# Kernel tuning notes

Measured on AMD Instinct MI355X. Metric: run time of the kernel, lower is better.

Reference implementation:

```python
import jax, jax.numpy as jnp
import numpy as np

B, T, D = 2, 2048, 1024
H, HS = 16, 64
EPS = 1e-5

def _ln(x, g, b):
    m = jnp.mean(x, axis=-1, keepdims=True)
    v = jnp.mean((x - m) ** 2, axis=-1, keepdims=True)
    return (x - m) * jax.lax.rsqrt(v + EPS) * g + b

def setup_inputs() -> dict:
    key = jax.random.key(0)
    ks = jax.random.split(key, 8)
    s_in = 1.0 / np.sqrt(D)
    s_ff = 1.0 / np.sqrt(4 * D)
    return {
        "embds": jax.random.normal(ks[0], (B, T, D), jnp.float32),
        "Wq": jax.random.normal(ks[1], (H, D, HS), jnp.float32) * s_in,
        "Wk": jax.random.normal(ks[2], (H, D, HS), jnp.float32) * s_in,
        "Wv": jax.random.normal(ks[3], (H, D, HS), jnp.float32) * s_in,
        "ln1_g": jnp.ones((D,), jnp.float32),
        "ln1_b": jnp.zeros((D,), jnp.float32),
        "ln2_g": jnp.ones((D,), jnp.float32),
        "ln2_b": jnp.zeros((D,), jnp.float32),
        "W1": jax.random.normal(ks[4], (D, 4 * D), jnp.float32) * s_in,
        "b1": jnp.zeros((4 * D,), jnp.float32),
        "W2": jax.random.normal(ks[5], (4 * D, D), jnp.float32) * s_ff,
        "b2": jnp.zeros((D,), jnp.float32),
    }

def reference(embds, Wq, Wk, Wv, ln1_g, ln1_b, ln2_g, ln2_b, W1, b1, W2, b2):
    _, t, d = embds.shape
    x = _ln(embds, ln1_g, ln1_b)
    q = jnp.einsum("btd,hde->bhte", x, Wq)
    k = jnp.einsum("btd,hde->bhte", x, Wk)
    v = jnp.einsum("btd,hde->bhte", x, Wv)
    # NOTE: repo scales by num_embds**-0.5 (C of input), not head_size**-0.5
    scores = jnp.einsum("bhte,bhse->bhts", q, k) * (d ** -0.5)
    causal = jnp.tril(jnp.ones((t, t), bool))
    scores = jnp.where(causal, scores, -jnp.inf)
    w = jax.nn.softmax(scores, axis=-1)
    o = jnp.einsum("bhts,bhse->bhte", w, v)  # [B,H,T,HS]
    attn = o.transpose(0, 2, 1, 3).reshape(embds.shape[0], t, -1)  # concat heads
    embds = embds + attn
    y = _ln(embds, ln2_g, ln2_b)
    ff = jax.nn.relu(y @ W1 + b1) @ W2 + b2
    return embds + ff
```

## Files before the change

kernel.cpp:

```cpp
#include <hip/hip_runtime.h>

using s16x8 = __attribute__((ext_vector_type(8))) short;
using f32x4 = __attribute__((ext_vector_type(4))) float;
typedef unsigned int   u32;
typedef unsigned short u16;

__device__ __forceinline__ u16 f2bf(float f) {
  u32 u = __float_as_uint(f);
  u += 0x7fffu + ((u >> 16) & 1u);
  return (u16)(u >> 16);
}
__device__ __forceinline__ float bf2f(u16 s) {
  return __uint_as_float(((u32)s) << 16);
}

typedef __attribute__((address_space(1))) const unsigned int g_u32;
typedef __attribute__((address_space(3))) unsigned int l_u32;
__device__ __forceinline__ void gload16(const void* g, void* l) {
  __builtin_amdgcn_global_load_lds((g_u32*)g, (l_u32*)l, 16, 0, 0);
}

#define WAITB(N) asm volatile("s_waitcnt vmcnt(" #N ")\ns_barrier" ::: "memory")
#define BAR()    asm volatile("s_barrier" ::: "memory")

__device__ __forceinline__ size_t kfrag_addr(int bh, int t, int e) {
  const int pair = (((t >> 4) & 3) << 1) + (e >> 5);
  const int slot = ((e >> 3) & 3) * 16 + (t & 15);
  return ((((size_t)bh * 32 + (t >> 6)) * 8 + pair) * 64 + slot) * 8 + (e & 7);
}
__device__ __forceinline__ size_t vfrag_addr(int bh, int t, int e) {
  const int pair = (((e >> 4) & 3) << 1) + ((t >> 5) & 1);
  const int slot = ((t >> 3) & 3) * 16 + (e & 15);
  return ((((size_t)bh * 32 + (t >> 6)) * 8 + pair) * 64 + slot) * 8 + (t & 7);
}

__global__ __launch_bounds__(256) void transpose_pack(
    const float* __restrict__ src, u16* __restrict__ dst, int R, int C)
{
  __shared__ u16 tile[64][66];
  const int tid = threadIdx.x;
  const int c0 = blockIdx.x * 64, r0 = blockIdx.y * 64;
  const size_t zoff = (size_t)blockIdx.z * R * C;
  src += zoff; dst += zoff;
  const int rr = tid >> 6, cc = tid & 63;
  #pragma unroll
  for (int i = 0; i < 16; ++i)
    tile[i * 4 + rr][cc] = f2bf(src[(size_t)(r0 + i * 4 + rr) * C + c0 + cc]);
  __syncthreads();
  #pragma unroll
  for (int i = 0; i < 16; ++i)
    dst[(size_t)(c0 + i * 4 + rr) * R + r0 + cc] = tile[cc][i * 4 + rr];
}

__global__ __launch_bounds__(256) void transpose_qkv(
    const float* __restrict__ Wq, const float* __restrict__ Wk,
    const float* __restrict__ Wv, u16* __restrict__ dst)
{
  __shared__ u16 tile[64][66];
  const int tid = threadIdx.x;
  const int sel = blockIdx.z >> 4, head = blockIdx.z & 15;
  const int r0 = blockIdx.y * 64;
  const float* src = ((sel == 0) ? Wq : (sel == 1) ? Wk : Wv) + (size_t)head * 65536;
  u16* d = dst + ((size_t)sel << 20) + (size_t)head * 65536;
  const int rr = tid >> 6, cc = tid & 63;
  #pragma unroll
  for (int i = 0; i < 16; ++i)
    tile[i * 4 + rr][cc] = f2bf(src[(size_t)(r0 + i * 4 + rr) * 64 + cc]);
  __syncthreads();
  #pragma unroll
  for (int i = 0; i < 16; ++i)
    d[(size_t)(i * 4 + rr) * 1024 + r0 + cc] = tile[cc][i * 4 + rr];
}

__global__ __launch_bounds__(256) void ln_kernel(
    const float* __restrict__ x, const float* __restrict__ g,
    const float* __restrict__ be, u16* __restrict__ out)
{
  const int row = blockIdx.x, tid = threadIdx.x;
  const int lane = tid & 63, wave = tid >> 6;
  const float4 v = ((const float4*)(x + (size_t)row * 1024))[tid];
  float s  = v.x + v.y + v.z + v.w;
  float sq = v.x * v.x + v.y * v.y + v.z * v.z + v.w * v.w;
  #pragma unroll
  for (int m = 1; m < 64; m <<= 1) { s += __shfl_xor(s, m); sq += __shfl_xor(sq, m); }
  __shared__ float rs[4], rq[4];
  if (lane == 0) { rs[wave] = s; rq[wave] = sq; }
  __syncthreads();
  s  = rs[0] + rs[1] + rs[2] + rs[3];
  sq = rq[0] + rq[1] + rq[2] + rq[3];
  const float mean = s * (1.0f / 1024.0f);
  const float var  = sq * (1.0f / 1024.0f) - mean * mean;
  const float rstd = rsqrtf(var + 1e-5f);
  const int c = tid * 4;
  const float4 gv = ((const float4*)g)[tid];
  const float4 bv = ((const float4*)be)[tid];
  ushort4 o;
  o.x = f2bf((v.x - mean) * rstd * gv.x + bv.x);
  o.y = f2bf((v.y - mean) * rstd * gv.y + bv.y);
  o.z = f2bf((v.z - mean) * rstd * gv.z + bv.z);
  o.w = f2bf((v.w - mean) * rstd * gv.w + bv.w);
  *(ushort4*)&out[(size_t)row * 1024 + c] = o;
}

#define MFMA_Q(MQ, NH)                                                        \
  do {                                                                        \
    __builtin_amdgcn_s_setprio(1);                                            \
    _Pragma("unroll") for (int m_ = 0; m_ < 4; ++m_)                          \
      _Pragma("unroll") for (int n_ = 0; n_ < 2; ++n_)                        \
        _Pragma("unroll") for (int ks_ = 0; ks_ < 2; ++ks_)                   \
          acc[MQ * 4 + m_][NH * 2 + n_] =                                     \
            __builtin_amdgcn_mfma_f32_16x16x32_bf16(                          \
              aF[m_][ks_], (NH ? b1F : b0F)[n_][ks_],                         \
              acc[MQ * 4 + m_][NH * 2 + n_], 0, 0, 0);                        \
    __builtin_amdgcn_s_setprio(0);                                            \
  } while (0)

template<int MODE>
__global__ __launch_bounds__(512, 2) void gemm256(
    const u16* __restrict__ A, int lda, const u16* __restrict__ BT, int ldb,
    int K, u16* __restrict__ o1, const float* __restrict__ bias,
    u16* __restrict__ pout, u16* __restrict__ o0q, u16* __restrict__ o0k,
    u16* __restrict__ o0v)
{
  __shared__ alignas(16) u16 lds[2][2][256 * 64];
  const int tid = threadIdx.x, lane = tid & 63, w = tid >> 6;
  const int wm = w >> 2, wn = w & 3;
  const int fr = lane & 15, g = lane >> 4;
  const int gx = gridDim.x, nwg = gx * gridDim.y;
  int lid = blockIdx.y * gx + blockIdx.x;
  lid = (lid & 7) * (nwg >> 3) + (lid >> 3);
  const int col0 = (lid % gx) * 256, row0 = (lid / gx) * 256;
  const int koff = (MODE == 3) ? blockIdx.z * 1024 : 0;
  if constexpr (MODE == 3) pout += (size_t)blockIdx.z * (4096 * 1024);

  const int srow = w * 16 + (lane >> 3);
  const int scol8 = (lane & 7) ^ ((lane >> 3) & 7);
  const u16* Ab = A  + (size_t)(row0 + srow) * lda + koff + scol8 * 8;
  const u16* Bb = BT + (size_t)(col0 + srow) * ldb + koff + scol8 * 8;
  const int sdst = (w * 16) * 64 + lane * 8;

  const int x7 = fr & 7;
  const int rA = wm * 128 + fr;
  const int rB = wn * 64 + fr;

  f32x4 acc[8][4] = {};
  s16x8 aF[4][2], b0F[2][2], b1F[2][2];
  const int nkt = K >> 6;

  auto stA = [&](int buf, int half, int kt) {
    #pragma unroll
    for (int g2 = 0; g2 < 2; ++g2)
      gload16(Ab + (size_t)(half * 128 + g2 * 8) * lda + kt * 64,
              &lds[buf][0][(half * 128 + g2 * 8) * 64 + sdst]);
  };
  auto stB = [&](int buf, int half, int kt) {
    #pragma unroll
    for (int g2 = 0; g2 < 2; ++g2)
      gload16(Bb + (size_t)(half * 128 + g2 * 8) * ldb + kt * 64,
              &lds[buf][1][(half * 128 + g2 * 8) * 64 + sdst]);
  };
  auto rdA = [&](int buf, int mq) {
    #pragma unroll
    for (int m = 0; m < 4; ++m)
      #pragma unroll
      for (int ks = 0; ks < 2; ++ks)
        aF[m][ks] = *(const s16x8*)
          &lds[buf][0][(rA + mq * 64 + m * 16) * 64 + ((ks * 4 + g) ^ x7) * 8];
  };
  auto rdB0 = [&](int buf) {
    #pragma unroll
    for (int n = 0; n < 2; ++n)
      #pragma unroll
      for (int ks = 0; ks < 2; ++ks)
        b0F[n][ks] = *(const s16x8*)
          &lds[buf][1][(rB + n * 16) * 64 + ((ks * 4 + g) ^ x7) * 8];
  };
  auto rdB1 = [&](int buf) {
    #pragma unroll
    for (int n = 0; n < 2; ++n)
      #pragma unroll
      for (int ks = 0; ks < 2; ++ks)
        b1F[n][ks] = *(const s16x8*)
          &lds[buf][1][(rB + (n + 2) * 16) * 64 + ((ks * 4 + g) ^ x7) * 8];
  };

  stA(0, 0, 0); stA(0, 1, 0); stB(0, 0, 0); stB(0, 1, 0);
  stA(1, 0, 1); stA(1, 1, 1); stB(1, 0, 1); stB(1, 1, 1);
  WAITB(8);

  const int niter = nkt >> 1;
  for (int i = 0; i < niter; ++i) {
    #pragma unroll
    for (int half = 0; half < 2; ++half) {
      const int buf = half;
      const int skt = 2 * i + 2 + half;
      const bool st = (skt < nkt);
      rdA(buf, 0); rdB0(buf);
      BAR();
      MFMA_Q(0, 0);
      BAR();
      rdB1(buf);
      if (st) stB(buf, 0, skt);
      BAR();
      MFMA_Q(0, 1);
      BAR();
      rdA(buf, 1);
      if (st) stA(buf, 0, skt);
      BAR();
      MFMA_Q(1, 0);
      BAR();
      if (st) { stA(buf, 1, skt); stB(buf, 1, skt); }
      BAR();
      MFMA_Q(1, 1);
      WAITB(6);
    }
  }

  const float QSCALE = 0.03125f * 1.4426950408889634f;
  #pragma unroll
  for (int m8 = 0; m8 < 8; ++m8) {
    const int rbase = row0 + wm * 128 + m8 * 16 + g * 4;
    #pragma unroll
    for (int n4 = 0; n4 < 4; ++n4) {
      const int col = col0 + wn * 64 + n4 * 16 + fr;
      if constexpr (MODE == 0) {
        const int ww = col >> 10, h = (col >> 6) & 15, e = col & 63;
        const int b = rbase >> 11, t0 = rbase & 2047;
        const int bh = b * 16 + h;
        if (ww == 0) {
          #pragma unroll
          for (int j = 0; j < 4; ++j)
            o0q[((size_t)bh * 2048 + (t0 + j)) * 64 + e] =
              f2bf(acc[m8][n4][j] * QSCALE);
        } else if (ww == 1) {
          #pragma unroll
          for (int j = 0; j < 4; ++j)
            o0k[kfrag_addr(bh, t0 + j, e)] = f2bf(acc[m8][n4][j]);
        } else {
          ushort4 pk;
          pk.x = f2bf(acc[m8][n4][0]); pk.y = f2bf(acc[m8][n4][1]);
          pk.z = f2bf(acc[m8][n4][2]); pk.w = f2bf(acc[m8][n4][3]);
          *(ushort4*)&o0v[vfrag_addr(bh, t0, e)] = pk;
        }
      } else if constexpr (MODE == 1) {
        const float bb = bias[col];
        #pragma unroll
        for (int j = 0; j < 4; ++j)
          o1[(size_t)(rbase + j) * 4096 + col] =
            f2bf(fmaxf(acc[m8][n4][j] + bb, 0.0f));
      } else {
        #pragma unroll
        for (int j = 0; j < 4; ++j)
          pout[(size_t)(rbase + j) * 1024 + col] = f2bf(acc[m8][n4][j]);
      }
    }
  }
}

__global__ __launch_bounds__(256) void ff2_reduce(
    const u16* __restrict__ pbuf, const float* __restrict__ e2,
    const float* __restrict__ b2, float* __restrict__ out)
{
  const int i4 = blockIdx.x * 256 + threadIdx.x;
  const int row = i4 >> 8, c4 = i4 & 255;
  float4 a = ((const float4*)e2)[i4];
  const float4 bb = ((const float4*)b2)[c4];
  a.x += bb.x; a.y += bb.y; a.z += bb.z; a.w += bb.w;
  #pragma unroll
  for (int z = 0; z < 4; ++z) {
    const ushort4 p = *(const ushort4*)
      &pbuf[(size_t)z * (4096 * 1024) + (size_t)row * 1024 + c4 * 4];
    a.x += bf2f(p.x); a.y += bf2f(p.y); a.z += bf2f(p.z); a.w += bf2f(p.w);
  }
  ((float4*)out)[i4] = a;
}

__global__ __launch_bounds__(256, 2) void attn_mfma(
    const u16* __restrict__ q, const u16* __restrict__ kfragG,
    const u16* __restrict__ vfragG, const float* __restrict__ embds,
    float* __restrict__ e2)
{
  __shared__ alignas(16) u16 kbuf[2][4096];
  __shared__ alignas(16) u16 vbuf[2][4096];
  __shared__ alignas(16) u16 p_sm[8][16][68];
  const int tid = threadIdx.x, lane = tid & 63, wave = tid >> 6;
  const int bh = blockIdx.x & 31;
  const int qb = 15 - (blockIdx.x >> 5);
  const int q0 = qb * 128 + wave * 32;
  const int b = bh >> 4, h = bh & 15;
  const int fr = lane & 15, g = lane >> 4;

  s16x8 qf[2][2];
  #pragma unroll
  for (int u = 0; u < 2; ++u) {
    const u16* qp = q + ((size_t)bh * 2048 + q0 + u * 16 + fr) * 64 + g * 8;
    qf[u][0] = *(const s16x8*)(qp);
    qf[u][1] = *(const s16x8*)(qp + 32);
  }

  f32x4 o_acc[2][4] = {};
  float lacc[2][4] = {};

  const size_t fragbase = (size_t)bh * 131072;
  const int nch = qb * 2 + 2;

  auto stage_kv = [&](int sel, int c) {
    const size_t cb = fragbase + (size_t)c * 4096;
    gload16(kfragG + cb + (wave * 2 + 0) * 512 + lane * 8, &kbuf[sel][(wave * 2 + 0) * 512]);
    gload16(kfragG + cb + (wave * 2 + 1) * 512 + lane * 8, &kbuf[sel][(wave * 2 + 1) * 512]);
    gload16(vfragG + cb + (wave * 2 + 0) * 512 + lane * 8, &vbuf[sel][(wave * 2 + 0) * 512]);
    gload16(vfragG + cb + (wave * 2 + 1) * 512 + lane * 8, &vbuf[sel][(wave * 2 + 1) * 512]);
  };

  auto compute = [&](int sel, int s0) {
    s16x8 kf[4][2];
    #pragma unroll
    for (int n = 0; n < 4; ++n)
      #pragma unroll
      for (int ks = 0; ks < 2; ++ks)
        kf[n][ks] = *(const s16x8*)&kbuf[sel][(n * 2 + ks) * 512 + lane * 8];

    #pragma unroll
    for (int u = 0; u < 2; ++u) {
      const int q0u = q0 + u * 16;
      f32x4 sacc[4] = {};
      #pragma unroll
      for (int n = 0; n < 4; ++n) {
        sacc[n] = __builtin_amdgcn_mfma_f32_16x16x32_bf16(qf[u][0], kf[n][0], sacc[n], 0, 0, 0);
        sacc[n] = __builtin_amdgcn_mfma_f32_16x16x32_bf16(qf[u][1], kf[n][1], sacc[n], 0, 0, 0);
      }
      if (s0 + 63 > q0u) {
        #pragma unroll
        for (int n = 0; n < 4; ++n) {
          const int s = s0 + n * 16 + fr;
          #pragma unroll
          for (int j = 0; j < 4; ++j)
            if (s > q0u + g * 4 + j) sacc[n][j] = -1e30f;
        }
      }
      #pragma unroll
      for (int n = 0; n < 4; ++n)
        #pragma unroll
        for (int j = 0; j < 4; ++j) {
          const float pe = __builtin_amdgcn_exp2f(sacc[n][j]);
          lacc[u][j] += pe;
          p_sm[wave * 2 + u][g * 4 + j][n * 16 + fr] = f2bf(pe);
        }
    }

    s16x8 vf[4][2];
    #pragma unroll
    for (int n = 0; n < 4; ++n)
      #pragma unroll
      for (int ks = 0; ks < 2; ++ks)
        vf[n][ks] = *(const s16x8*)&vbuf[sel][(n * 2 + ks) * 512 + lane * 8];

    #pragma unroll
    for (int u = 0; u < 2; ++u) {
      const s16x8 pf0 = *(const s16x8*)&p_sm[wave * 2 + u][fr][g * 8];
      const s16x8 pf1 = *(const s16x8*)&p_sm[wave * 2 + u][fr][32 + g * 8];
      #pragma unroll
      for (int n = 0; n < 4; ++n) {
        o_acc[u][n] = __builtin_amdgcn_mfma_f32_16x16x32_bf16(pf0, vf[n][0], o_acc[u][n], 0, 0, 0);
        o_acc[u][n] = __builtin_amdgcn_mfma_f32_16x16x32_bf16(pf1, vf[n][1], o_acc[u][n], 0, 0, 0);
      }
    }
  };

  stage_kv(0, 0);
  for (int t = 0; t < nch; ++t) {
    WAITB(0);
    if (t + 1 < nch) stage_kv((t + 1) & 1, t + 1);
    compute(t & 1, t * 64);
  }

  #pragma unroll
  for (int u = 0; u < 2; ++u)
    #pragma unroll
    for (int j = 0; j < 4; ++j) {
      #pragma unroll
      for (int mm = 1; mm < 16; mm <<= 1) lacc[u][j] += __shfl_xor(lacc[u][j], mm);
    }

  #pragma unroll
  for (int u = 0; u < 2; ++u)
    #pragma unroll
    for (int n = 0; n < 4; ++n) {
      #pragma unroll
      for (int j = 0; j < 4; ++j) {
        const int t = q0 + u * 16 + g * 4 + j;
        const size_t oi = ((size_t)b * 2048 + t) * 1024 + (size_t)h * 64 + n * 16 + fr;
        e2[oi] = embds[oi] + o_acc[u][n][j] / lacc[u][j];
      }
    }
}

extern "C" void kernel_launch(void* const* d_in, const int* in_sizes, int n_in,
                              void* d_out, int out_size, void* d_ws, size_t ws_size,
                              hipStream_t stream) {
  const float* embds = (const float*)d_in[0];
  const float* Wq    = (const float*)d_in[1];
  const float* Wk    = (const float*)d_in[2];
  const float* Wv    = (const float*)d_in[3];
  const float* ln1g  = (const float*)d_in[4];
  const float* ln1b  = (const float*)d_in[5];
  const float* ln2g  = (const float*)d_in[6];
  const float* ln2b  = (const float*)d_in[7];
  const float* W1    = (const float*)d_in[8];
  const float* b1    = (const float*)d_in[9];
  const float* W2    = (const float*)d_in[10];
  const float* b2    = (const float*)d_in[11];
  float* out = (float*)d_out;

  char* ws = (char*)d_ws;
  u16*   xln   = (u16*)(ws);
  u16*   pbuf  = (u16*)(ws);
  u16*   wqkvT = (u16*)(ws + (8ull  << 20));
  u16*   qbuf  = (u16*)(ws + (14ull << 20));
  u16*   kfrag = (u16*)(ws + (22ull << 20));
  u16*   vfrag = (u16*)(ws + (30ull << 20));
  float* e2    = (float*)(ws + (38ull << 20));
  u16*   ybuf  = (u16*)(ws + (54ull << 20));
  u16*   w1T   = (u16*)(ws + (62ull << 20));
  u16*   w2T   = (u16*)(ws + (70ull << 20));
  u16*   hid   = (u16*)(ws + (78ull << 20));

  transpose_qkv<<<dim3(1, 16, 48), 256, 0, stream>>>(Wq, Wk, Wv, wqkvT);
  transpose_pack<<<dim3(64, 16, 1), 256, 0, stream>>>(W1, w1T, 1024, 4096);
  transpose_pack<<<dim3(16, 64, 1), 256, 0, stream>>>(W2, w2T, 4096, 1024);
  ln_kernel<<<4096, 256, 0, stream>>>(embds, ln1g, ln1b, xln);
  gemm256<0><<<dim3(12, 16), 512, 0, stream>>>(xln, 1024, wqkvT, 1024, 1024,
      nullptr, nullptr, nullptr, qbuf, kfrag, vfrag);
  attn_mfma<<<512, 256, 0, stream>>>(qbuf, kfrag, vfrag, embds, e2);
  ln_kernel<<<4096, 256, 0, stream>>>(e2, ln2g, ln2b, ybuf);
  gemm256<1><<<dim3(16, 16), 512, 0, stream>>>(ybuf, 1024, w1T, 1024, 1024,
      hid, b1, nullptr, nullptr, nullptr, nullptr);
  gemm256<3><<<dim3(4, 16, 4), 512, 0, stream>>>(hid, 4096, w2T, 4096, 1024,
      nullptr, nullptr, pbuf, nullptr, nullptr, nullptr);
  ff2_reduce<<<4096, 256, 0, stream>>>(pbuf, e2, b2, out);
}
```

Measured before the change: 196.7 us.

## Load K/V fragments directly into registers with register double-buffering

```diff
diff --git a/kernel.cpp b/kernel.cpp
--- a/kernel.cpp
+++ b/kernel.cpp
@@ -280,9 +280,7 @@
     const u16* __restrict__ vfragG, const float* __restrict__ embds,
     float* __restrict__ e2)
 {
-  __shared__ alignas(16) u16 kbuf[2][4096];
-  __shared__ alignas(16) u16 vbuf[2][4096];
-  __shared__ alignas(16) u16 p_sm[8][16][68];
+  __shared__ alignas(16) u16 p_sm[4][16][68];
   const int tid = threadIdx.x, lane = tid & 63, wave = tid >> 6;
   const int bh = blockIdx.x & 31;
   const int qb = 15 - (blockIdx.x >> 5);
@@ -302,32 +300,29 @@
   float lacc[2][4] = {};
 
   const size_t fragbase = (size_t)bh * 131072;
+  const u16* kb = kfragG + fragbase + lane * 8;
+  const u16* vb = vfragG + fragbase + lane * 8;
   const int nch = qb * 2 + 2;
 
-  auto stage_kv = [&](int sel, int c) {
-    const size_t cb = fragbase + (size_t)c * 4096;
-    gload16(kfragG + cb + (wave * 2 + 0) * 512 + lane * 8, &kbuf[sel][(wave * 2 + 0) * 512]);
-    gload16(kfragG + cb + (wave * 2 + 1) * 512 + lane * 8, &kbuf[sel][(wave * 2 + 1) * 512]);
-    gload16(vfragG + cb + (wave * 2 + 0) * 512 + lane * 8, &vbuf[sel][(wave * 2 + 0) * 512]);
-    gload16(vfragG + cb + (wave * 2 + 1) * 512 + lane * 8, &vbuf[sel][(wave * 2 + 1) * 512]);
-  };
-
-  auto compute = [&](int sel, int s0) {
-    s16x8 kf[4][2];
-    #pragma unroll
-    for (int n = 0; n < 4; ++n)
-      #pragma unroll
-      for (int ks = 0; ks < 2; ++ks)
-        kf[n][ks] = *(const s16x8*)&kbuf[sel][(n * 2 + ks) * 512 + lane * 8];
-
+  auto loadKV = [&](s16x8 (&kd)[8], s16x8 (&vd)[8], int c) {
+    const u16* kc = kb + (size_t)c * 4096;
+    const u16* vc = vb + (size_t)c * 4096;
+    #pragma unroll
+    for (int p = 0; p < 8; ++p) {
+      kd[p] = *(const s16x8*)(kc + p * 512);
+      vd[p] = *(const s16x8*)(vc + p * 512);
+    }
+  };
+
+  auto compute = [&](const s16x8 (&kf)[8], const s16x8 (&vf)[8], int s0) {
     #pragma unroll
     for (int u = 0; u < 2; ++u) {
       const int q0u = q0 + u * 16;
       f32x4 sacc[4] = {};
       #pragma unroll
       for (int n = 0; n < 4; ++n) {
-        sacc[n] = __builtin_amdgcn_mfma_f32_16x16x32_bf16(qf[u][0], kf[n][0], sacc[n], 0, 0, 0);
-        sacc[n] = __builtin_amdgcn_mfma_f32_16x16x32_bf16(qf[u][1], kf[n][1], sacc[n], 0, 0, 0);
+        sacc[n] = __builtin_amdgcn_mfma_f32_16x16x32_bf16(qf[u][0], kf[n * 2 + 0], sacc[n], 0, 0, 0);
+        sacc[n] = __builtin_amdgcn_mfma_f32_16x16x32_bf16(qf[u][1], kf[n * 2 + 1], sacc[n], 0, 0, 0);
       }
       if (s0 + 63 > q0u) {
         #pragma unroll
@@ -344,34 +339,25 @@
         for (int j = 0; j < 4; ++j) {
           const float pe = __builtin_amdgcn_exp2f(sacc[n][j]);
           lacc[u][j] += pe;
-          p_sm[wave * 2 + u][g * 4 + j][n * 16 + fr] = f2bf(pe);
+          p_sm[wave][g * 4 + j][n * 16 + fr] = f2bf(pe);
         }
-    }
-
-    s16x8 vf[4][2];
-    #pragma unroll
-    for (int n = 0; n < 4; ++n)
-      #pragma unroll
-      for (int ks = 0; ks < 2; ++ks)
-        vf[n][ks] = *(const s16x8*)&vbuf[sel][(n * 2 + ks) * 512 + lane * 8];
-
-    #pragma unroll
-    for (int u = 0; u < 2; ++u) {
-      const s16x8 pf0 = *(const s16x8*)&p_sm[wave * 2 + u][fr][g * 8];
-      const s16x8 pf1 = *(const s16x8*)&p_sm[wave * 2 + u][fr][32 + g * 8];
+      const s16x8 pf0 = *(const s16x8*)&p_sm[wave][fr][g * 8];
+      const s16x8 pf1 = *(const s16x8*)&p_sm[wave][fr][32 + g * 8];
       #pragma unroll
       for (int n = 0; n < 4; ++n) {
-        o_acc[u][n] = __builtin_amdgcn_mfma_f32_16x16x32_bf16(pf0, vf[n][0], o_acc[u][n], 0, 0, 0);
-        o_acc[u][n] = __builtin_amdgcn_mfma_f32_16x16x32_bf16(pf1, vf[n][1], o_acc[u][n], 0, 0, 0);
+        o_acc[u][n] = __builtin_amdgcn_mfma_f32_16x16x32_bf16(pf0, vf[n * 2 + 0], o_acc[u][n], 0, 0, 0);
+        o_acc[u][n] = __builtin_amdgcn_mfma_f32_16x16x32_bf16(pf1, vf[n * 2 + 1], o_acc[u][n], 0, 0, 0);
       }
     }
   };
 
-  stage_kv(0, 0);
-  for (int t = 0; t < nch; ++t) {
-    WAITB(0);
-    if (t + 1 < nch) stage_kv((t + 1) & 1, t + 1);
-    compute(t & 1, t * 64);
+  s16x8 kA[8], vA[8], kB[8], vB[8];
+  loadKV(kA, vA, 0);
+  for (int t = 0; t < nch; t += 2) {
+    loadKV(kB, vB, t + 1);
+    compute(kA, vA, t * 64);
+    if (t + 2 < nch) loadKV(kA, vA, t + 2);
+    compute(kB, vB, (t + 1) * 64);
   }
 
   #pragma unroll
```

New measurement: 201.0 us. 1.02x slower.
